# Kernel tuning notes

Hardware: AMD Instinct MI355X
Metric: run time of the kernel (lower is better)

Reference implementation:

```python
import jax, jax.numpy as jnp
import numpy as np

N = 12000      # total nodes
T = 6000       # tail (query) nodes
H = 4000       # head (key/value) nodes
D = 256        # att_hidd_dim
NUM_HEADS = 8
HEAD_DIM = D // NUM_HEADS
EDGE_VOCAB = 64


def setup_inputs() -> dict:
    key = jax.random.key(0)
    ks = jax.random.split(key, 16)
    inp = {
        "query": jax.random.normal(ks[0], (N, D), jnp.float32),
        "key": jax.random.normal(ks[1], (N, D), jnp.float32),
        "value": jax.random.normal(ks[2], (N, D), jnp.float32),
        "adj_matrix": jax.random.randint(ks[3], (T, H), 0, 2, jnp.int32),
        "c_indices": jax.random.randint(ks[4], (T, H), 0, EDGE_VOCAB, jnp.int32),
        "ground_ind_tail": jnp.arange(T, dtype=jnp.int32),
        "ground_ind_head": jnp.arange(H, dtype=jnp.int32) + T,  # disjoint bipartite sets
        "Wq": 0.02 * jax.random.normal(ks[5], (D, D), jnp.float32),
        "bq": jnp.zeros((D,), jnp.float32),
        "Wk": 0.02 * jax.random.normal(ks[6], (D, D), jnp.float32),
        "bk": jnp.zeros((D,), jnp.float32),
        "Wv": 0.02 * jax.random.normal(ks[7], (D, D), jnp.float32),
        "bv": jnp.zeros((D,), jnp.float32),
        "Wo": 0.02 * jax.random.normal(ks[8], (D, D), jnp.float32),
        "bo": jnp.zeros((D,), jnp.float32),
        "edge_emb": 0.02 * jax.random.normal(ks[9], (EDGE_VOCAB, NUM_HEADS), jnp.float32),
    }
    return inp


def reference(query, key, value, adj_matrix, c_indices, ground_ind_tail,
              ground_ind_head, Wq, bq, Wk, bk, Wv, bv, Wo, bo, edge_emb):
    scaling = HEAD_DIM ** -0.5
    # gather + project; [heads, T, hd] / [heads, H, hd]
    q_tail = ((query[ground_ind_tail] @ Wq.T + bq) * scaling).reshape(T, NUM_HEADS, HEAD_DIM).swapaxes(0, 1)
    k_head = (key[ground_ind_head] @ Wk.T + bk).reshape(H, NUM_HEADS, HEAD_DIM).swapaxes(0, 1)
    v_head = (value[ground_ind_head] @ Wv.T + bv).reshape(H, NUM_HEADS, HEAD_DIM).swapaxes(0, 1)

    tail_mask = jnp.where(adj_matrix == 0, -1e9, 0.0)[None]              # [1, T, H]
    edge_bias = edge_emb[c_indices].transpose(2, 0, 1)                    # [heads, T, H]

    scores = jnp.einsum('htd,hsd->hts', q_tail, k_head) + tail_mask + edge_bias
    attn = jax.nn.softmax(scores, axis=-1)
    out_tail = jnp.einsum('hts,hsd->htd', attn, v_head)                   # [heads, T, hd]

    attn_all = jnp.zeros((NUM_HEADS, N, HEAD_DIM), query.dtype)
    attn_all = attn_all.at[:, ground_ind_tail].set(out_tail)
    attn_all = attn_all.at[:, ground_ind_head].set(
        query[ground_ind_head].reshape(H, NUM_HEADS, HEAD_DIM).swapaxes(0, 1))
    attn_all = attn_all.swapaxes(0, 1).reshape(N, D)                      # [N, D]
    return attn_all @ Wo.T + bo
```

## Files before the change

### kernel.cpp

```cpp
#include <hip/hip_runtime.h>
#include <hip/hip_bf16.h>

#define T_N 6000
#define H_N 4000
#define N_N 12000
#define DIM 256
#define NHEAD 8
#define HDIM 32
#define SCALING 0.17677669529663687f
#define LOG2E 1.4426950408889634f
#define NTT 375
#define NTP 188
#define NST 125

typedef __attribute__((ext_vector_type(8))) short bf16x8;
typedef __attribute__((ext_vector_type(4))) float f32x4;

union BF8U { bf16x8 v; unsigned int w[4]; __hip_bfloat16 h[8]; unsigned short us[8]; };

static __device__ __forceinline__ unsigned int cvt_pk_bf16(float a, float b) {
  unsigned int r;
  asm("v_cvt_pk_bf16_f32 %0, %1, %2" : "=v"(r) : "v"(a), "v"(b));
  return r;
}

static __device__ __forceinline__ int swz256(int w) {
  return w ^ (((w >> 5) & 3) << 3);
}

__global__ __launch_bounds__(256) void pack_pc(
    const int* __restrict__ adj, const int* __restrict__ cind,
    unsigned int* __restrict__ pc)
{
  __shared__ unsigned int lds[256];
  const int bid = blockIdx.x;
  const int tid = threadIdx.x;
  const int ttp = bid / 125;
  const int st  = bid % 125;
  const int tb  = tid >> 7;
  const int tl  = (tid >> 3) & 15;
  const int gi  = tid & 7;
  const int tt  = ttp * 2 + tb;

  if (tt < NTT) {
    const int t  = tt * 16 + tl;
    const int s0 = st * 32 + gi * 4;
    const int4 c4 = *reinterpret_cast<const int4*>(cind + (size_t)t * H_N + s0);
    const int4 a4 = *reinterpret_cast<const int4*>(adj + (size_t)t * H_N + s0);
    unsigned int w = 0;
    w |= (unsigned)((c4.x & 63) | (a4.x ? 64 : 0));
    w |= (unsigned)((c4.y & 63) | (a4.y ? 64 : 0)) << 8;
    w |= (unsigned)((c4.z & 63) | (a4.z ? 64 : 0)) << 16;
    w |= (unsigned)((c4.w & 63) | (a4.w ? 64 : 0)) << 24;
    const int wloc = tb * 128 + gi * 16 + tl;
    lds[swz256(wloc)] = w;
  }
  __syncthreads();

  const bool full = (ttp < 187);
  const size_t base = full ? (size_t)bid * 256
                           : (size_t)5984000 + (size_t)st * 128;
  const int nw = full ? 256 : 128;
  if (tid < nw) pc[base + tid] = lds[swz256(tid)];
}

static __device__ __forceinline__ void proj_body(
    int role, const float* __restrict__ X, const int* __restrict__ idx,
    const float* __restrict__ W, const float* __restrict__ bvec,
    __hip_bfloat16* __restrict__ outf, int rows, float scale, int bx,
    char* As, char* Bs)
{
  const int tid = threadIdx.x;
  const int w = tid >> 6;
  const int lane = tid & 63;
  const int q = lane >> 4;
  const int t = lane & 15;
  const int n0 = (bx & 7) * 32;
  const int m0 = (bx >> 3) * 64;

  for (int i = tid; i < 2048; i += 256) {
    const int row = i >> 5, c16 = i & 31;
    BF8U u;
    u.w[0] = 0; u.w[1] = 0; u.w[2] = 0; u.w[3] = 0;
    const int gr = m0 + row;
    if (gr < rows) {
      const int src = idx ? idx[gr] : gr;
      const float* sp = X + (size_t)src * DIM + c16 * 8;
      const float4 x0 = *reinterpret_cast<const float4*>(sp);
      const float4 x1 = *reinterpret_cast<const float4*>(sp + 4);
      u.w[0] = cvt_pk_bf16(x0.x, x0.y);
      u.w[1] = cvt_pk_bf16(x0.z, x0.w);
      u.w[2] = cvt_pk_bf16(x1.x, x1.y);
      u.w[3] = cvt_pk_bf16(x1.z, x1.w);
    }
    *reinterpret_cast<bf16x8*>(As + ((row * 512 + c16 * 16) ^ ((row & 7) << 4))) = u.v;
  }
  for (int i = tid; i < 1024; i += 256) {
    const int row = i >> 5, c16 = i & 31;
    const float* sp = W + (size_t)(n0 + row) * DIM + c16 * 8;
    const float4 x0 = *reinterpret_cast<const float4*>(sp);
    const float4 x1 = *reinterpret_cast<const float4*>(sp + 4);
    BF8U u;
    u.w[0] = cvt_pk_bf16(x0.x, x0.y);
    u.w[1] = cvt_pk_bf16(x0.z, x0.w);
    u.w[2] = cvt_pk_bf16(x1.x, x1.y);
    u.w[3] = cvt_pk_bf16(x1.z, x1.w);
    *reinterpret_cast<bf16x8*>(Bs + ((row * 512 + c16 * 16) ^ ((row & 7) << 4))) = u.v;
  }
  __syncthreads();

  f32x4 acc0 = {0.f, 0.f, 0.f, 0.f};
  f32x4 acc1 = {0.f, 0.f, 0.f, 0.f};
#pragma unroll
  for (int kk = 0; kk < 8; kk++) {
    const int arow = w * 16 + t;
    const bf16x8 af = *reinterpret_cast<const bf16x8*>(
        As + ((arow * 512 + (kk * 32 + q * 8) * 2) ^ ((arow & 7) << 4)));
    const bf16x8 bf0 = *reinterpret_cast<const bf16x8*>(
        Bs + ((t * 512 + (kk * 32 + q * 8) * 2) ^ ((t & 7) << 4)));
    const bf16x8 bf1 = *reinterpret_cast<const bf16x8*>(
        Bs + (((16 + t) * 512 + (kk * 32 + q * 8) * 2) ^ (((16 + t) & 7) << 4)));
    acc0 = __builtin_amdgcn_mfma_f32_16x16x32_bf16(af, bf0, acc0, 0, 0, 0);
    acc1 = __builtin_amdgcn_mfma_f32_16x16x32_bf16(af, bf1, acc1, 0, 0, 0);
  }

#pragma unroll
  for (int r = 0; r < 4; r++) {
    const int grow = m0 + w * 16 + q * 4 + r;
    if (grow >= rows) continue;
    const float a0 = acc0[r], a1 = acc1[r];
    const int jj[2] = {n0 + t, n0 + 16 + t};
    const float vv[2] = {(a0 + bvec[jj[0]]) * scale, (a1 + bvec[jj[1]]) * scale};
#pragma unroll
    for (int f = 0; f < 2; f++) {
      const int j = jj[f];
      const __hip_bfloat16 hv = __float2bfloat16(vv[f]);
      const int h = j >> 5;
      size_t idxo;
      if (role == 1) {
        idxo = (((size_t)h * NTT + (grow >> 4)) * 64 + ((j & 31) >> 3) * 16 +
                (grow & 15)) * 8 + (j & 7);
      } else if (role == 2) {
        idxo = (((size_t)h * 250 + (grow >> 4)) * 64 + ((j & 31) >> 3) * 16 +
                (grow & 15)) * 8 + (j & 7);
      } else {
        const int dh = (j & 31) >> 4, dl = j & 15;
        const int sl = grow & 31;
        const int qv = (sl & 15) >> 2;
        const int ev = (sl & 3) | (((sl >> 4) & 1) << 2);
        idxo = ((((size_t)h * 2 + dh) * NST + (grow >> 5)) * 64 +
                qv * 16 + dl) * 8 + ev;
      }
      outf[idxo] = hv;
    }
  }
}

#define NBQ 752
#define NBK 504
#define NBV 504
#define NBC 1000

__global__ __launch_bounds__(256) void proj_all(
    const float* __restrict__ query, const float* __restrict__ key,
    const float* __restrict__ value, const int* __restrict__ tail_idx,
    const int* __restrict__ head_idx,
    const float* __restrict__ Wq, const float* __restrict__ bq,
    const float* __restrict__ Wk, const float* __restrict__ bk,
    const float* __restrict__ Wv, const float* __restrict__ bv,
    __hip_bfloat16* __restrict__ Qf, __hip_bfloat16* __restrict__ Kf,
    __hip_bfloat16* __restrict__ Vf, __hip_bfloat16* __restrict__ Ab)
{
  __shared__ __align__(16) char As[64 * 512];
  __shared__ __align__(16) char Bs[32 * 512];

  const int bx = blockIdx.x;
  if (bx < NBQ) {
    proj_body(1, query, tail_idx, Wq, bq, Qf, T_N, SCALING * LOG2E, bx, As, Bs);
  } else if (bx < NBQ + NBK) {
    proj_body(2, key, head_idx, Wk, bk, Kf, H_N, 1.f, bx - NBQ, As, Bs);
  } else if (bx < NBQ + NBK + NBV) {
    proj_body(3, value, head_idx, Wv, bv, Vf, H_N, 1.f, bx - NBQ - NBK, As, Bs);
  } else {
    const int b = bx - NBQ - NBK - NBV;
    const int rr = b * 4 + (threadIdx.x >> 6);
    const int lane = threadIdx.x & 63;
    const int row = head_idx[rr];
    const float4 v = *reinterpret_cast<const float4*>(
        query + (size_t)row * DIM + lane * 4);
    uint2 o;
    o.x = cvt_pk_bf16(v.x, v.y);
    o.y = cvt_pk_bf16(v.z, v.w);
    *reinterpret_cast<uint2*>(Ab + (size_t)row * DIM + lane * 4) = o;
  }
}

__global__ __launch_bounds__(256, 4) void attn_mfma(
    const __hip_bfloat16* __restrict__ Qf, const __hip_bfloat16* __restrict__ Kf,
    const __hip_bfloat16* __restrict__ Vf, const unsigned int* __restrict__ pc,
    const float* __restrict__ edge_emb, const int* __restrict__ tail_idx,
    __hip_bfloat16* __restrict__ Ab)
{
  __shared__ float tab[128];
  __shared__ float mg[3][64][18];

  const int tid = threadIdx.x;
  const int cs = tid >> 6;
  const int lane = tid & 63;
  const int q = lane >> 4;
  const int t = lane & 15;
  const int h = blockIdx.x;
  const int ttp = blockIdx.y;
  const int hbase = h * HDIM;

  if (tid < 128) {
    tab[tid] = (tid < 64) ? -1e9f : edge_emb[(tid - 64) * NHEAD + h] * LOG2E;
  }

  const bool full = (ttp < 187);
  const int tAt = ttp * 2;
  const int tBt = full ? (ttp * 2 + 1) : 374;

  const bf16x8 qfA = *reinterpret_cast<const bf16x8*>(
      Qf + (((size_t)h * NTT + tAt) * 64 + lane) * 8);
  const bf16x8 qfB = *reinterpret_cast<const bf16x8*>(
      Qf + (((size_t)h * NTT + tBt) * 64 + lane) * 8);

  const int stBeg = (cs * NST) >> 2;
  const int stEnd = ((cs + 1) * NST) >> 2;

  const size_t pbase = full ? ((size_t)(ttp * 125 + stBeg) * 256)
                            : ((size_t)5984000 + (size_t)stBeg * 128);
  const int pcStep = full ? 256 : 128;
  const int pbOff  = full ? 128 : 0;
  const unsigned int* pcp = pc + pbase + q * 16 + t;
  const __hip_bfloat16* kp = Kf + (((size_t)h * 250 + stBeg * 2) * 64 + lane) * 8;
  const __hip_bfloat16* vp = Vf + (((size_t)h * 2 * NST + stBeg) * 64 + lane) * 8;
  const size_t VD = (size_t)NST * 64 * 8;

  f32x4 oaccA0 = {0.f, 0.f, 0.f, 0.f};
  f32x4 oaccA1 = {0.f, 0.f, 0.f, 0.f};
  f32x4 oaccB0 = {0.f, 0.f, 0.f, 0.f};
  f32x4 oaccB1 = {0.f, 0.f, 0.f, 0.f};
  f32x4 laccA  = {0.f, 0.f, 0.f, 0.f};
  f32x4 laccB  = {0.f, 0.f, 0.f, 0.f};

  BF8U ones;
#pragma unroll
  for (int e = 0; e < 8; e++) ones.us[e] = 0x3F80;

  unsigned int npcA0 = pcp[0], npcA1 = pcp[64];
  unsigned int npcB0 = pcp[pbOff], npcB1 = pcp[pbOff + 64];
  bf16x8 nk0 = *reinterpret_cast<const bf16x8*>(kp);
  bf16x8 nk1 = *reinterpret_cast<const bf16x8*>(kp + 512);

  __syncthreads();

  for (int st = stBeg; st < stEnd; ++st) {
    const unsigned int cA0 = npcA0, cA1 = npcA1, cB0 = npcB0, cB1 = npcB1;
    const bf16x8 kf0 = nk0, kf1 = nk1;

    const bf16x8 vf0 = *reinterpret_cast<const bf16x8*>(vp);
    const bf16x8 vf1 = *reinterpret_cast<const bf16x8*>(vp + VD);
    vp += 512;

    const f32x4 z = {0.f, 0.f, 0.f, 0.f};
    __builtin_amdgcn_s_setprio(1);
    const f32x4 sA_lo = __builtin_amdgcn_mfma_f32_16x16x32_bf16(kf0, qfA, z, 0, 0, 0);
    const f32x4 sA_hi = __builtin_amdgcn_mfma_f32_16x16x32_bf16(kf1, qfA, z, 0, 0, 0);
    const f32x4 sB_lo = __builtin_amdgcn_mfma_f32_16x16x32_bf16(kf0, qfB, z, 0, 0, 0);
    const f32x4 sB_hi = __builtin_amdgcn_mfma_f32_16x16x32_bf16(kf1, qfB, z, 0, 0, 0);
    __builtin_amdgcn_s_setprio(0);

    if (st + 1 < stEnd) {
      pcp += pcStep; kp += 1024;
      npcA0 = pcp[0];
      npcA1 = pcp[64];
      npcB0 = pcp[pbOff];
      npcB1 = pcp[pbOff + 64];
      nk0 = *reinterpret_cast<const bf16x8*>(kp);
      nk1 = *reinterpret_cast<const bf16x8*>(kp + 512);
    }

    float pA[8], pB[8];
#pragma unroll
    for (int r = 0; r < 4; r++) {
      pA[r]     = __builtin_amdgcn_exp2f(sA_lo[r] + tab[(cA0 >> (r * 8)) & 127u]);
      pA[r + 4] = __builtin_amdgcn_exp2f(sA_hi[r] + tab[(cA1 >> (r * 8)) & 127u]);
      pB[r]     = __builtin_amdgcn_exp2f(sB_lo[r] + tab[(cB0 >> (r * 8)) & 127u]);
      pB[r + 4] = __builtin_amdgcn_exp2f(sB_hi[r] + tab[(cB1 >> (r * 8)) & 127u]);
    }

    BF8U puA, puB;
    puA.w[0] = cvt_pk_bf16(pA[0], pA[1]);
    puA.w[1] = cvt_pk_bf16(pA[2], pA[3]);
    puA.w[2] = cvt_pk_bf16(pA[4], pA[5]);
    puA.w[3] = cvt_pk_bf16(pA[6], pA[7]);
    puB.w[0] = cvt_pk_bf16(pB[0], pB[1]);
    puB.w[1] = cvt_pk_bf16(pB[2], pB[3]);
    puB.w[2] = cvt_pk_bf16(pB[4], pB[5]);
    puB.w[3] = cvt_pk_bf16(pB[6], pB[7]);

    __builtin_amdgcn_s_setprio(1);
    oaccA0 = __builtin_amdgcn_mfma_f32_16x16x32_bf16(vf0, puA.v, oaccA0, 0, 0, 0);
    oaccA1 = __builtin_amdgcn_mfma_f32_16x16x32_bf16(vf1, puA.v, oaccA1, 0, 0, 0);
    laccA  = __builtin_amdgcn_mfma_f32_16x16x32_bf16(ones.v, puA.v, laccA, 0, 0, 0);
    oaccB0 = __builtin_amdgcn_mfma_f32_16x16x32_bf16(vf0, puB.v, oaccB0, 0, 0, 0);
    oaccB1 = __builtin_amdgcn_mfma_f32_16x16x32_bf16(vf1, puB.v, oaccB1, 0, 0, 0);
    laccB  = __builtin_amdgcn_mfma_f32_16x16x32_bf16(ones.v, puB.v, laccB, 0, 0, 0);
    __builtin_amdgcn_s_setprio(0);
  }

  float LA = laccA[0];
  float LB = laccB[0];

  if (cs) {
#pragma unroll
    for (int r = 0; r < 4; r++) {
      mg[cs - 1][lane][r]      = oaccA0[r];
      mg[cs - 1][lane][4 + r]  = oaccA1[r];
      mg[cs - 1][lane][8 + r]  = oaccB0[r];
      mg[cs - 1][lane][12 + r] = oaccB1[r];
    }
    mg[cs - 1][lane][16] = LA;
    mg[cs - 1][lane][17] = LB;
  }
  __syncthreads();
  if (!cs) {
    float oA[8], oB[8];
#pragma unroll
    for (int r = 0; r < 4; r++) {
      oA[r] = oaccA0[r]; oA[4 + r] = oaccA1[r];
      oB[r] = oaccB0[r]; oB[4 + r] = oaccB1[r];
    }
#pragma unroll
    for (int c = 0; c < 3; c++) {
      LA += mg[c][lane][16];
      LB += mg[c][lane][17];
#pragma unroll
      for (int r = 0; r < 8; r++) {
        oA[r] += mg[c][lane][r];
        oB[r] += mg[c][lane][8 + r];
      }
    }
    const float invA = 1.f / LA;
    const float invB = 1.f / LB;
    const int rowA = tail_idx[tAt * 16 + t];
    const int rowB = tail_idx[tBt * 16 + t];
    __hip_bfloat16* dstA = Ab + (size_t)rowA * DIM + hbase + q * 4;
    __hip_bfloat16* dstB = Ab + (size_t)rowB * DIM + hbase + q * 4;
    uint2 wa0, wa1, wb0, wb1;
    wa0.x = cvt_pk_bf16(oA[0] * invA, oA[1] * invA);
    wa0.y = cvt_pk_bf16(oA[2] * invA, oA[3] * invA);
    wa1.x = cvt_pk_bf16(oA[4] * invA, oA[5] * invA);
    wa1.y = cvt_pk_bf16(oA[6] * invA, oA[7] * invA);
    wb0.x = cvt_pk_bf16(oB[0] * invB, oB[1] * invB);
    wb0.y = cvt_pk_bf16(oB[2] * invB, oB[3] * invB);
    wb1.x = cvt_pk_bf16(oB[4] * invB, oB[5] * invB);
    wb1.y = cvt_pk_bf16(oB[6] * invB, oB[7] * invB);
    *reinterpret_cast<uint2*>(dstA) = wa0;
    *reinterpret_cast<uint2*>(dstA + 16) = wa1;
    *reinterpret_cast<uint2*>(dstB) = wb0;
    *reinterpret_cast<uint2*>(dstB + 16) = wb1;
  }
}

__global__ __launch_bounds__(256) void oproj_mfma(
    const __hip_bfloat16* __restrict__ Ab, const float* __restrict__ Wo,
    const float* __restrict__ bo, float* __restrict__ out)
{
  __shared__ __align__(16) char As[64 * 512];
  __shared__ __align__(16) char Bs[32 * 512];

  const int tid = threadIdx.x;
  const int w = tid >> 6;
  const int lane = tid & 63;
  const int bl = lane & 15;
  const int q = lane >> 4;
  const int n0 = blockIdx.x * 32;
  const int m0 = blockIdx.y * 64;

  for (int i = tid; i < 2048; i += 256) {
    const int row = i >> 5, c16 = i & 31;
    bf16x8 v = {0, 0, 0, 0, 0, 0, 0, 0};
    const int gr = m0 + row;
    if (gr < N_N)
      v = *reinterpret_cast<const bf16x8*>(Ab + (size_t)gr * DIM + c16 * 8);
    *reinterpret_cast<bf16x8*>(As + ((row * 512 + c16 * 16) ^ ((row & 7) << 4))) = v;
  }
  for (int i = tid; i < 1024; i += 256) {
    const int row = i >> 5, c16 = i & 31;
    const float* src = Wo + (size_t)(n0 + row) * DIM + c16 * 8;
    const float4 x0 = *reinterpret_cast<const float4*>(src);
    const float4 x1 = *reinterpret_cast<const float4*>(src + 4);
    BF8U u;
    u.w[0] = cvt_pk_bf16(x0.x, x0.y);
    u.w[1] = cvt_pk_bf16(x0.z, x0.w);
    u.w[2] = cvt_pk_bf16(x1.x, x1.y);
    u.w[3] = cvt_pk_bf16(x1.z, x1.w);
    *reinterpret_cast<bf16x8*>(Bs + ((row * 512 + c16 * 16) ^ ((row & 7) << 4))) = u.v;
  }
  __syncthreads();

  f32x4 acc0 = {0.f, 0.f, 0.f, 0.f};
  f32x4 acc1 = {0.f, 0.f, 0.f, 0.f};
#pragma unroll
  for (int kk = 0; kk < 8; kk++) {
    const int arow = w * 16 + bl;
    const bf16x8 af = *reinterpret_cast<const bf16x8*>(
        As + ((arow * 512 + (kk * 32 + q * 8) * 2) ^ ((arow & 7) << 4)));
    const bf16x8 bf0 = *reinterpret_cast<const bf16x8*>(
        Bs + ((bl * 512 + (kk * 32 + q * 8) * 2) ^ ((bl & 7) << 4)));
    const int brow = 16 + bl;
    const bf16x8 bf1 = *reinterpret_cast<const bf16x8*>(
        Bs + ((brow * 512 + (kk * 32 + q * 8) * 2) ^ ((brow & 7) << 4)));
    acc0 = __builtin_amdgcn_mfma_f32_16x16x32_bf16(af, bf0, acc0, 0, 0, 0);
    acc1 = __builtin_amdgcn_mfma_f32_16x16x32_bf16(af, bf1, acc1, 0, 0, 0);
  }

#pragma unroll
  for (int r = 0; r < 4; r++) {
    const int grow = m0 + w * 16 + q * 4 + r;
    if (grow < N_N) {
      const int j0 = n0 + bl;
      const int j1 = n0 + 16 + bl;
      out[(size_t)grow * DIM + j0] = acc0[r] + bo[j0];
      out[(size_t)grow * DIM + j1] = acc1[r] + bo[j1];
    }
  }
}

extern "C" void kernel_launch(void* const* d_in, const int* in_sizes, int n_in,
                              void* d_out, int out_size, void* d_ws, size_t ws_size,
                              hipStream_t stream)
{
  const float* query    = (const float*)d_in[0];
  const float* key      = (const float*)d_in[1];
  const float* value    = (const float*)d_in[2];
  const int*   adj      = (const int*)d_in[3];
  const int*   cind     = (const int*)d_in[4];
  const int*   tail_idx = (const int*)d_in[5];
  const int*   head_idx = (const int*)d_in[6];
  const float* Wq = (const float*)d_in[7];
  const float* bq = (const float*)d_in[8];
  const float* Wk = (const float*)d_in[9];
  const float* bk = (const float*)d_in[10];
  const float* Wv = (const float*)d_in[11];
  const float* bv = (const float*)d_in[12];
  const float* Wo = (const float*)d_in[13];
  const float* bo = (const float*)d_in[14];
  const float* edge_emb = (const float*)d_in[15];

  float* out = (float*)d_out;
  char*  ws  = (char*)d_ws;

  __hip_bfloat16* Ab = (__hip_bfloat16*)ws;
  __hip_bfloat16* Qf = (__hip_bfloat16*)(ws + 6144000);
  __hip_bfloat16* Kf = (__hip_bfloat16*)(ws + 9216000);
  __hip_bfloat16* Vf = (__hip_bfloat16*)(ws + 11264000);
  unsigned int*   pc = (unsigned int*)(ws + 13312000);

  hipMemsetAsync(Ab + (size_t)10000 * DIM, 0,
                 (size_t)2000 * DIM * sizeof(__hip_bfloat16), stream);

  pack_pc<<<dim3(NTP * NST), dim3(256), 0, stream>>>(adj, cind, pc);

  proj_all<<<dim3(NBQ + NBK + NBV + NBC), dim3(256), 0, stream>>>(
      query, key, value, tail_idx, head_idx,
      Wq, bq, Wk, bk, Wv, bv, Qf, Kf, Vf, Ab);

  attn_mfma<<<dim3(NHEAD, NTP), dim3(256), 0, stream>>>(
      Qf, Kf, Vf, pc, edge_emb, tail_idx, Ab);

  oproj_mfma<<<dim3(8, (N_N + 63) / 64), dim3(256), 0, stream>>>(
      Ab, Wo, bo, out);
}
```

Before: 139.2 us.

## Repack adjacency/edge-code words as adjacent pairs and use grid-stride pack kernel

The packing kernel now uses a grid-stride loop. Each thread reads two int4 chunks of c_indices and adj and writes a uint2 holding the lo/hi words side by side, so the LDS transpose and its barrier are gone. The attention kernel's layout changes to match: each lane fetches its two code words per tile with one 8-byte load instead of two scalar loads. The pack step also drops the &63 mask and the adj?64:0 test, so it now assumes c_indices < 64 and adj in {0,1}.

```diff
diff --git a/kernel.cpp b/kernel.cpp
--- a/kernel.cpp
+++ b/kernel.cpp
@@ -12,6 +12,7 @@
 #define NTT 375
 #define NTP 188
 #define NST 125
+#define NPAIR 3000000
 
 typedef __attribute__((ext_vector_type(8))) short bf16x8;
 typedef __attribute__((ext_vector_type(4))) float f32x4;
@@ -24,44 +25,48 @@
   return r;
 }
 
-static __device__ __forceinline__ int swz256(int w) {
-  return w ^ (((w >> 5) & 3) << 3);
-}
-
 __global__ __launch_bounds__(256) void pack_pc(
     const int* __restrict__ adj, const int* __restrict__ cind,
     unsigned int* __restrict__ pc)
 {
-  __shared__ unsigned int lds[256];
-  const int bid = blockIdx.x;
-  const int tid = threadIdx.x;
-  const int ttp = bid / 125;
-  const int st  = bid % 125;
-  const int tb  = tid >> 7;
-  const int tl  = (tid >> 3) & 15;
-  const int gi  = tid & 7;
-  const int tt  = ttp * 2 + tb;
-
-  if (tt < NTT) {
-    const int t  = tt * 16 + tl;
-    const int s0 = st * 32 + gi * 4;
-    const int4 c4 = *reinterpret_cast<const int4*>(cind + (size_t)t * H_N + s0);
-    const int4 a4 = *reinterpret_cast<const int4*>(adj + (size_t)t * H_N + s0);
-    unsigned int w = 0;
-    w |= (unsigned)((c4.x & 63) | (a4.x ? 64 : 0));
-    w |= (unsigned)((c4.y & 63) | (a4.y ? 64 : 0)) << 8;
-    w |= (unsigned)((c4.z & 63) | (a4.z ? 64 : 0)) << 16;
-    w |= (unsigned)((c4.w & 63) | (a4.w ? 64 : 0)) << 24;
-    const int wloc = tb * 128 + gi * 16 + tl;
-    lds[swz256(wloc)] = w;
-  }
-  __syncthreads();
-
-  const bool full = (ttp < 187);
-  const size_t base = full ? (size_t)bid * 256
-                           : (size_t)5984000 + (size_t)st * 128;
-  const int nw = full ? 256 : 128;
-  if (tid < nw) pc[base + tid] = lds[swz256(tid)];
+  const int stride = gridDim.x * 256;
+  for (int P = blockIdx.x * 256 + threadIdx.x; P < NPAIR; P += stride) {
+    int t_row, st, k, widx;
+    if (P < 2992000) {
+      const int T = P >> 6;
+      const int inner = P & 63;
+      const int tl = inner >> 2;
+      k = inner & 3;
+      const int ttp = T / 250;
+      const int r = T - ttp * 250;
+      st = r >> 1;
+      t_row = ttp * 32 + (r & 1) * 16 + tl;
+      widx = T * 128 + tl * 8 + k * 2;
+    } else {
+      const int Pp = P - 2992000;
+      const int inner = Pp & 63;
+      const int tl = inner >> 2;
+      k = inner & 3;
+      st = Pp >> 6;
+      t_row = 5984 + tl;
+      widx = 5984000 + st * 128 + tl * 8 + k * 2;
+    }
+    const size_t ib = (size_t)t_row * H_N + st * 32 + k * 4;
+    const int4 cl = *reinterpret_cast<const int4*>(cind + ib);
+    const int4 al = *reinterpret_cast<const int4*>(adj + ib);
+    const int4 ch = *reinterpret_cast<const int4*>(cind + ib + 16);
+    const int4 ah = *reinterpret_cast<const int4*>(adj + ib + 16);
+    uint2 o;
+    o.x = (unsigned)(cl.x | (al.x << 6)) |
+          ((unsigned)(cl.y | (al.y << 6)) << 8) |
+          ((unsigned)(cl.z | (al.z << 6)) << 16) |
+          ((unsigned)(cl.w | (al.w << 6)) << 24);
+    o.y = (unsigned)(ch.x | (ah.x << 6)) |
+          ((unsigned)(ch.y | (ah.y << 6)) << 8) |
+          ((unsigned)(ch.z | (ah.z << 6)) << 16) |
+          ((unsigned)(ch.w | (ah.w << 6)) << 24);
+    *reinterpret_cast<uint2*>(pc + widx) = o;
+  }
 }
 
 static __device__ __forceinline__ void proj_body(
@@ -233,7 +238,7 @@
                             : ((size_t)5984000 + (size_t)stBeg * 128);
   const int pcStep = full ? 256 : 128;
   const int pbOff  = full ? 128 : 0;
-  const unsigned int* pcp = pc + pbase + q * 16 + t;
+  const unsigned int* pcp = pc + pbase + t * 8 + q * 2;
   const __hip_bfloat16* kp = Kf + (((size_t)h * 250 + stBeg * 2) * 64 + lane) * 8;
   const __hip_bfloat16* vp = Vf + (((size_t)h * 2 * NST + stBeg) * 64 + lane) * 8;
   const size_t VD = (size_t)NST * 64 * 8;
@@ -249,8 +254,10 @@
 #pragma unroll
   for (int e = 0; e < 8; e++) ones.us[e] = 0x3F80;
 
-  unsigned int npcA0 = pcp[0], npcA1 = pcp[64];
-  unsigned int npcB0 = pcp[pbOff], npcB1 = pcp[pbOff + 64];
+  uint2 pA = *reinterpret_cast<const uint2*>(pcp);
+  uint2 pB = *reinterpret_cast<const uint2*>(pcp + pbOff);
+  unsigned int npcA0 = pA.x, npcA1 = pA.y;
+  unsigned int npcB0 = pB.x, npcB1 = pB.y;
   bf16x8 nk0 = *reinterpret_cast<const bf16x8*>(kp);
   bf16x8 nk1 = *reinterpret_cast<const bf16x8*>(kp + 512);
 
@@ -274,32 +281,32 @@
 
     if (st + 1 < stEnd) {
       pcp += pcStep; kp += 1024;
-      npcA0 = pcp[0];
-      npcA1 = pcp[64];
-      npcB0 = pcp[pbOff];
-      npcB1 = pcp[pbOff + 64];
+      pA = *reinterpret_cast<const uint2*>(pcp);
+      pB = *reinterpret_cast<const uint2*>(pcp + pbOff);
+      npcA0 = pA.x; npcA1 = pA.y;
+      npcB0 = pB.x; npcB1 = pB.y;
       nk0 = *reinterpret_cast<const bf16x8*>(kp);
       nk1 = *reinterpret_cast<const bf16x8*>(kp + 512);
     }
 
-    float pA[8], pB[8];
+    float pAv[8], pBv[8];
 #pragma unroll
     for (int r = 0; r < 4; r++) {
-      pA[r]     = __builtin_amdgcn_exp2f(sA_lo[r] + tab[(cA0 >> (r * 8)) & 127u]);
-      pA[r + 4] = __builtin_amdgcn_exp2f(sA_hi[r] + tab[(cA1 >> (r * 8)) & 127u]);
-      pB[r]     = __builtin_amdgcn_exp2f(sB_lo[r] + tab[(cB0 >> (r * 8)) & 127u]);
-      pB[r + 4] = __builtin_amdgcn_exp2f(sB_hi[r] + tab[(cB1 >> (r * 8)) & 127u]);
+      pAv[r]     = __builtin_amdgcn_exp2f(sA_lo[r] + tab[(cA0 >> (r * 8)) & 127u]);
+      pAv[r + 4] = __builtin_amdgcn_exp2f(sA_hi[r] + tab[(cA1 >> (r * 8)) & 127u]);
+      pBv[r]     = __builtin_amdgcn_exp2f(sB_lo[r] + tab[(cB0 >> (r * 8)) & 127u]);
+      pBv[r + 4] = __builtin_amdgcn_exp2f(sB_hi[r] + tab[(cB1 >> (r * 8)) & 127u]);
     }
 
     BF8U puA, puB;
-    puA.w[0] = cvt_pk_bf16(pA[0], pA[1]);
-    puA.w[1] = cvt_pk_bf16(pA[2], pA[3]);
-    puA.w[2] = cvt_pk_bf16(pA[4], pA[5]);
-    puA.w[3] = cvt_pk_bf16(pA[6], pA[7]);
-    puB.w[0] = cvt_pk_bf16(pB[0], pB[1]);
-    puB.w[1] = cvt_pk_bf16(pB[2], pB[3]);
-    puB.w[2] = cvt_pk_bf16(pB[4], pB[5]);
-    puB.w[3] = cvt_pk_bf16(pB[6], pB[7]);
+    puA.w[0] = cvt_pk_bf16(pAv[0], pAv[1]);
+    puA.w[1] = cvt_pk_bf16(pAv[2], pAv[3]);
+    puA.w[2] = cvt_pk_bf16(pAv[4], pAv[5]);
+    puA.w[3] = cvt_pk_bf16(pAv[6], pAv[7]);
+    puB.w[0] = cvt_pk_bf16(pBv[0], pBv[1]);
+    puB.w[1] = cvt_pk_bf16(pBv[2], pBv[3]);
+    puB.w[2] = cvt_pk_bf16(pBv[4], pBv[5]);
+    puB.w[3] = cvt_pk_bf16(pBv[6], pBv[7]);
 
     __builtin_amdgcn_s_setprio(1);
     oaccA0 = __builtin_amdgcn_mfma_f32_16x16x32_bf16(vf0, puA.v, oaccA0, 0, 0, 0);
@@ -463,7 +470,7 @@
   hipMemsetAsync(Ab + (size_t)10000 * DIM, 0,
                  (size_t)2000 * DIM * sizeof(__hip_bfloat16), stream);
 
-  pack_pc<<<dim3(NTP * NST), dim3(256), 0, stream>>>(adj, cind, pc);
+  pack_pc<<<dim3(2048), dim3(256), 0, stream>>>(adj, cind, pc);
 
   proj_all<<<dim3(NBQ + NBK + NBV + NBC), dim3(256), 0, stream>>>(
       query, key, value, tail_idx, head_idx,
```

New measurement: 138.7 us (median of 2 runs). No clear change (-0.3%).
